# Performance work log

Measured on AMD Instinct MI355X. Metric: run time of the kernel, lower is better.

The kernel has to match this reference:

```python
import jax, jax.numpy as jnp
import numpy as np
import math

HIDDEN = 1024
HEADS = 16
HEAD_DIM = HIDDEN // HEADS
B, S = 2, 2048


def _xavier(key, shape):
    fan_in, fan_out = shape[1], shape[0]
    limit = math.sqrt(6.0 / (fan_in + fan_out))
    return jax.random.uniform(key, shape, jnp.float32, -limit, limit)


def setup_inputs() -> dict:
    key = jax.random.key(0)
    ks = jax.random.split(key, 5)
    x = jax.random.normal(ks[0], (B, S, HIDDEN), jnp.float32)
    # torch Linear stores weight as [out, in]; y = x @ W.T + b
    Wq = _xavier(ks[1], (HIDDEN, HIDDEN))
    Wk = _xavier(ks[2], (HIDDEN, HIDDEN))
    Wv = _xavier(ks[3], (HIDDEN, HIDDEN))
    Wo = _xavier(ks[4], (HIDDEN, HIDDEN))
    bq = jnp.zeros((HIDDEN,), jnp.float32)
    bk = jnp.zeros((HIDDEN,), jnp.float32)
    bv = jnp.zeros((HIDDEN,), jnp.float32)
    bo = jnp.zeros((HIDDEN,), jnp.float32)
    return {"x": x, "Wq": Wq, "bq": bq, "Wk": Wk, "bk": bk,
            "Wv": Wv, "bv": bv, "Wo": Wo, "bo": bo}


def reference(x, Wq, bq, Wk, bk, Wv, bv, Wo, bo):
    b, s, d = x.shape
    h, hd = HEADS, HEAD_DIM
    q = (x @ Wq.T + bq).reshape(b, s, h, hd).transpose(0, 2, 1, 3)  # [b,h,s,hd]
    k = (x @ Wk.T + bk).reshape(b, s, h, hd).transpose(0, 2, 1, 3)
    v = (x @ Wv.T + bv).reshape(b, s, h, hd).transpose(0, 2, 1, 3)
    scores = jnp.einsum('bhqd,bhkd->bhqk', q, k) / math.sqrt(hd)
    causal = jnp.tril(jnp.ones((s, s), bool))
    scores = jnp.where(causal, scores, -jnp.inf)
    attn = jax.nn.softmax(scores, axis=-1)
    out = jnp.einsum('bhqk,bhkd->bhqd', attn, v)  # [b,h,s,hd]
    out = out.transpose(0, 2, 1, 3).reshape(b, s, d)
    return out @ Wo.T + bo
```

## Files before the change

### kernel.cpp

```cpp
#include <hip/hip_runtime.h>
#include <hip/hip_bf16.h>


typedef __hip_bfloat16 bf16;
typedef __attribute__((ext_vector_type(8))) short short8;
typedef __attribute__((ext_vector_type(4))) short short4v;
typedef __attribute__((ext_vector_type(4))) float f32x4;

#define MFMA16(a, b, c) __builtin_amdgcn_mfma_f32_16x16x32_bf16((a), (b), (c), 0, 0, 0)

__device__ __forceinline__ void load_lds16(const void* g, void* l) {
  __builtin_amdgcn_global_load_lds(
      (const __attribute__((address_space(1))) void*)g,
      (__attribute__((address_space(3))) void*)l, 16, 0, 0);
}

__global__ __launch_bounds__(256) void cvt_kernel(
    const float* __restrict__ x, const float* __restrict__ wq,
    const float* __restrict__ wk, const float* __restrict__ wv,
    const float* __restrict__ wo, bf16* __restrict__ xb, bf16* __restrict__ wqb,
    bf16* __restrict__ wkb, bf16* __restrict__ wvb, bf16* __restrict__ wob) {
  const int seg = blockIdx.y;
  const float* src;
  bf16* dst;
  int n;
  if (seg == 0)      { src = x;  dst = xb;  n = 4194304; }
  else if (seg == 1) { src = wq; dst = wqb; n = 1048576; }
  else if (seg == 2) { src = wk; dst = wkb; n = 1048576; }
  else if (seg == 3) { src = wv; dst = wvb; n = 1048576; }
  else               { src = wo; dst = wob; n = 1048576; }
  const int i = (blockIdx.x * 256 + threadIdx.x) * 4;
  if (i >= n) return;
  const float4 v = *(const float4*)(src + i);
  short4v p;
  ((bf16*)&p)[0] = __float2bfloat16(v.x);
  ((bf16*)&p)[1] = __float2bfloat16(v.y);
  ((bf16*)&p)[2] = __float2bfloat16(v.z);
  ((bf16*)&p)[3] = __float2bfloat16(v.w);
  *(short4v*)(dst + i) = p;
}

template <typename OutT>
__device__ __forceinline__ void gemm_body(const bf16* __restrict__ X,
                                          const bf16* __restrict__ W,
                                          const float* __restrict__ bias,
                                          OutT* __restrict__ Y, float scale) {
  constexpr int K = 1024, N = 1024;
  __shared__ bf16 As[128 * 32];
  __shared__ bf16 Bs[128 * 32];
  const int t = threadIdx.x;
  const int lane = t & 63, w = t >> 6;
  const int quad = lane >> 4, r = lane & 15;
  const int m0 = blockIdx.y * 128, n0 = blockIdx.x * 128;
  const int wm = w >> 1, wn = w & 1;

  f32x4 acc[4][4] = {};

  for (int k0 = 0; k0 < K; k0 += 32) {
    __syncthreads();
#pragma unroll
    for (int p = 0; p < 2; ++p) {
      const int c = p * 256 + w * 64 + lane;
      const int row = c >> 2;
      const int scb = (c & 3) ^ ((row >> 1) & 3);
      load_lds16(X + (size_t)(m0 + row) * K + k0 + scb * 8,
                 As + (p * 256 + w * 64) * 8);
      load_lds16(W + (size_t)(n0 + row) * K + k0 + scb * 8,
                 Bs + (p * 256 + w * 64) * 8);
    }
    __syncthreads();
    short8 af[4], bfr[4];
#pragma unroll
    for (int i = 0; i < 4; ++i) {
      const int ra = wm * 64 + i * 16 + r;
      af[i] = *(const short8*)(As + ra * 32 + ((quad ^ ((ra >> 1) & 3)) * 8));
      const int rb = wn * 64 + i * 16 + r;
      bfr[i] = *(const short8*)(Bs + rb * 32 + ((quad ^ ((rb >> 1) & 3)) * 8));
    }
#pragma unroll
    for (int i = 0; i < 4; ++i)
#pragma unroll
      for (int j = 0; j < 4; ++j)
        acc[i][j] = MFMA16(af[i], bfr[j], acc[i][j]);
  }
#pragma unroll
  for (int i = 0; i < 4; ++i) {
    const int m = m0 + wm * 64 + i * 16 + quad * 4;
#pragma unroll
    for (int j = 0; j < 4; ++j) {
      const int n = n0 + wn * 64 + j * 16 + r;
      const float bv = bias[n];
#pragma unroll
      for (int g = 0; g < 4; ++g) {
        const float val = (acc[i][j][g] + bv) * scale;
        if constexpr (__is_same(OutT, float))
          Y[(size_t)(m + g) * N + n] = val;
        else
          Y[(size_t)(m + g) * N + n] = __float2bfloat16(val);
      }
    }
  }
}

__global__ __launch_bounds__(256) void qkv_kernel(
    const bf16* __restrict__ x, const bf16* __restrict__ Wq,
    const float* __restrict__ bq, const bf16* __restrict__ Wk,
    const float* __restrict__ bk, const bf16* __restrict__ Wv,
    const float* __restrict__ bv, bf16* Qb, bf16* Kb, bf16* Vb) {
  const bf16* W;
  const float* bias;
  bf16* Y;
  float scale = 1.0f;
  if (blockIdx.z == 0) { W = Wq; bias = bq; Y = Qb; scale = 0.125f; }
  else if (blockIdx.z == 1) { W = Wk; bias = bk; Y = Kb; }
  else { W = Wv; bias = bv; Y = Vb; }
  gemm_body<bf16>(x, W, bias, Y, scale);
}

__global__ __launch_bounds__(256) void proj_kernel(const bf16* __restrict__ X,
                                                   const bf16* __restrict__ W,
                                                   const float* __restrict__ bias,
                                                   float* __restrict__ Y) {
  gemm_body<float>(X, W, bias, Y, 1.0f);
}

__global__ __launch_bounds__(256) void attn_kernel(const bf16* __restrict__ Qb,
                                                   const bf16* __restrict__ Kb,
                                                   const bf16* __restrict__ Vb,
                                                   bf16* __restrict__ Ob) {
  const int pair = blockIdx.x, h = blockIdx.y, b = blockIdx.z;
  const int t = threadIdx.x;
  const int lane = t & 63, w = t >> 6;
  const int quad = lane >> 4, r = lane & 15;

  __shared__ bf16 Ks[64 * 64];
  __shared__ bf16 Vt[64 * 64];
  __shared__ bf16 Pl[4][16 * 64];

#pragma unroll 1
  for (int sel = 0; sel < 2; ++sel) {
    const int j = sel ? (31 - pair) : pair;
    const int q0 = j * 64;
    const int qrow = q0 + w * 16 + r;

    short8 qf[2];
#pragma unroll
    for (int ks = 0; ks < 2; ++ks)
      qf[ks] = *(const short8*)(Qb + (size_t)(b * 2048 + qrow) * 1024 + h * 64 +
                                ks * 32 + quad * 8);

    f32x4 o[4] = {};
    float mrow = -1e30f, lrow = 0.f;

    for (int kt = 0; kt <= j; ++kt) {
      const int k0 = kt * 64;
      __syncthreads();
#pragma unroll
      for (int p = 0; p < 2; ++p) {
        const int c = p * 256 + w * 64 + lane;
        const int row = c >> 3;
        const int scb = (c & 7) ^ (row & 7);
        load_lds16(Kb + (size_t)(b * 2048 + k0 + row) * 1024 + h * 64 + scb * 8,
                   Ks + (p * 256 + w * 64) * 8);
      }
      {
        const bf16* vsrc =
            Vb + (size_t)(b * 2048 + k0 + lane) * 1024 + h * 64 + w * 16;
        short8 v0 = *(const short8*)(vsrc);
        short8 v1 = *(const short8*)(vsrc + 8);
        const int s8 = lane >> 3, s7 = lane & 7;
#pragma unroll
        for (int jj = 0; jj < 8; ++jj) {
          const int d0 = w * 16 + jj, d1 = w * 16 + 8 + jj;
          Vt[d0 * 64 + ((s8 ^ jj) * 8) + s7] = ((const bf16*)&v0)[jj];
          Vt[d1 * 64 + ((s8 ^ jj) * 8) + s7] = ((const bf16*)&v1)[jj];
        }
      }
      __syncthreads();

      f32x4 st[4] = {};
#pragma unroll
      for (int ks = 0; ks < 2; ++ks) {
        short8 kf[4];
#pragma unroll
        for (int mt = 0; mt < 4; ++mt) {
          const int key = mt * 16 + r;
          kf[mt] = *(const short8*)(Ks + key * 64 +
                                    (((ks * 4 + quad) ^ (key & 7)) * 8));
        }
#pragma unroll
        for (int mt = 0; mt < 4; ++mt) st[mt] = MFMA16(kf[mt], qf[ks], st[mt]);
      }

      if (kt == j) {
#pragma unroll
        for (int mt = 0; mt < 4; ++mt)
#pragma unroll
          for (int g = 0; g < 4; ++g) {
            const int key = k0 + mt * 16 + quad * 4 + g;
            if (key > qrow) st[mt][g] = -1e30f;
          }
      }

      float mx = -1e30f;
#pragma unroll
      for (int mt = 0; mt < 4; ++mt)
#pragma unroll
        for (int g = 0; g < 4; ++g) mx = fmaxf(mx, st[mt][g]);
      mx = fmaxf(mx, __shfl_xor(mx, 16));
      mx = fmaxf(mx, __shfl_xor(mx, 32));
      const float mnew = fmaxf(mrow, mx);
      const float alpha = __expf(mrow - mnew);
      mrow = mnew;
      float sum = 0.f;
#pragma unroll
      for (int mt = 0; mt < 4; ++mt) {
        bf16 pk[4];
#pragma unroll
        for (int g = 0; g < 4; ++g) {
          const float p = __expf(st[mt][g] - mnew);
          pk[g] = __float2bfloat16(p);
          sum += __bfloat162float(pk[g]);
        }
        const int key8 = mt * 2 + (quad >> 1);
        const int off = r * 64 + ((key8 ^ (r & 7)) * 8) + (quad & 1) * 4;
        *(short4v*)(&Pl[w][off]) = *(const short4v*)pk;
      }
      sum += __shfl_xor(sum, 16);
      sum += __shfl_xor(sum, 32);
      lrow = lrow * alpha + sum;
#pragma unroll
      for (int mt = 0; mt < 4; ++mt)
#pragma unroll
        for (int g = 0; g < 4; ++g) o[mt][g] *= alpha;

      asm volatile("s_waitcnt lgkmcnt(0)" ::: "memory");

#pragma unroll
      for (int ks = 0; ks < 2; ++ks) {
        short8 vf[4], pf;
#pragma unroll
        for (int mt = 0; mt < 4; ++mt) {
          const int d = mt * 16 + r;
          vf[mt] = *(const short8*)(Vt + d * 64 +
                                    (((ks * 4 + quad) ^ (d & 7)) * 8));
        }
        pf = *(const short8*)(Pl[w] + r * 64 + (((ks * 4 + quad) ^ (r & 7)) * 8));
#pragma unroll
        for (int mt = 0; mt < 4; ++mt) o[mt] = MFMA16(vf[mt], pf, o[mt]);
      }
    }

    const float inv = 1.f / lrow;
#pragma unroll
    for (int mt = 0; mt < 4; ++mt) {
      const int d0 = mt * 16 + quad * 4;
      short4v pk;
#pragma unroll
      for (int g = 0; g < 4; ++g)
        ((bf16*)&pk)[g] = __float2bfloat16(o[mt][g] * inv);
      *(short4v*)(Ob + (size_t)(b * 2048 + qrow) * 1024 + h * 64 + d0) = pk;
    }
  }
}

extern "C" void kernel_launch(void* const* d_in, const int* in_sizes, int n_in,
                              void* d_out, int out_size, void* d_ws, size_t ws_size,
                              hipStream_t stream) {
  const float* x  = (const float*)d_in[0];
  const float* Wq = (const float*)d_in[1];
  const float* bq = (const float*)d_in[2];
  const float* Wk = (const float*)d_in[3];
  const float* bk = (const float*)d_in[4];
  const float* Wv = (const float*)d_in[5];
  const float* bv = (const float*)d_in[6];
  const float* Wo = (const float*)d_in[7];
  const float* bo = (const float*)d_in[8];
  float* out = (float*)d_out;

  bf16* xb  = (bf16*)d_ws;
  bf16* wqb = xb  + (size_t)4096 * 1024;
  bf16* wkb = wqb + (size_t)1024 * 1024;
  bf16* wvb = wkb + (size_t)1024 * 1024;
  bf16* wob = wvb + (size_t)1024 * 1024;
  bf16* Qb  = wob + (size_t)1024 * 1024;
  bf16* Kb  = Qb  + (size_t)4096 * 1024;
  bf16* Vb  = Kb  + (size_t)4096 * 1024;
  bf16* Ob  = Vb  + (size_t)4096 * 1024;
  const size_t need = ((size_t)4096 * 1024 * 5 + (size_t)1024 * 1024 * 4) * 2;
  if (ws_size < need) return;

  cvt_kernel<<<dim3(4096, 5), 256, 0, stream>>>(x, Wq, Wk, Wv, Wo,
                                                xb, wqb, wkb, wvb, wob);
  qkv_kernel<<<dim3(8, 32, 3), 256, 0, stream>>>(xb, wqb, bq, wkb, bk, wvb, bv,
                                                 Qb, Kb, Vb);
  attn_kernel<<<dim3(16, 16, 2), 256, 0, stream>>>(Qb, Kb, Vb, Ob);
  proj_kernel<<<dim3(8, 32, 1), 256, 0, stream>>>(Ob, wob, bo, out);
}
```

Measured before the change: 206.3 us.

## Split attention into one block per query tile, shrink proj tile, use exp2

The attention kernel no longer pairs a short and a long causal query tile per block. It launches one block per 64-row tile, heaviest tiles first, which doubles the grid and gives the scheduler finer load balancing. The output projection now uses a 64-row M tile so it launches twice as many blocks. Q is pre-scaled by log2(e)/sqrt(d) so softmax can use exp2f instead of __expf. Each block now does less work, so each block also spends a larger share of its time loading Q and running its prologue.

```diff
diff --git a/kernel.cpp b/kernel.cpp
--- a/kernel.cpp
+++ b/kernel.cpp
@@ -40,52 +40,60 @@
   *(short4v*)(dst + i) = p;
 }
 
-template <typename OutT>
+template <int BM, typename OutT>
 __device__ __forceinline__ void gemm_body(const bf16* __restrict__ X,
                                           const bf16* __restrict__ W,
                                           const float* __restrict__ bias,
                                           OutT* __restrict__ Y, float scale) {
   constexpr int K = 1024, N = 1024;
-  __shared__ bf16 As[128 * 32];
+  constexpr int MI = BM / 32;
+  __shared__ bf16 As[BM * 32];
   __shared__ bf16 Bs[128 * 32];
   const int t = threadIdx.x;
   const int lane = t & 63, w = t >> 6;
   const int quad = lane >> 4, r = lane & 15;
-  const int m0 = blockIdx.y * 128, n0 = blockIdx.x * 128;
+  const int m0 = blockIdx.y * BM, n0 = blockIdx.x * 128;
   const int wm = w >> 1, wn = w & 1;
 
-  f32x4 acc[4][4] = {};
+  f32x4 acc[MI][4] = {};
 
   for (int k0 = 0; k0 < K; k0 += 32) {
     __syncthreads();
+#pragma unroll
+    for (int p = 0; p < BM / 64; ++p) {
+      const int c = p * 256 + w * 64 + lane;
+      const int row = c >> 2;
+      const int scb = (c & 3) ^ ((row >> 1) & 3);
+      load_lds16(X + (size_t)(m0 + row) * K + k0 + scb * 8, As + c * 8);
+    }
 #pragma unroll
     for (int p = 0; p < 2; ++p) {
       const int c = p * 256 + w * 64 + lane;
       const int row = c >> 2;
       const int scb = (c & 3) ^ ((row >> 1) & 3);
-      load_lds16(X + (size_t)(m0 + row) * K + k0 + scb * 8,
-                 As + (p * 256 + w * 64) * 8);
-      load_lds16(W + (size_t)(n0 + row) * K + k0 + scb * 8,
-                 Bs + (p * 256 + w * 64) * 8);
+      load_lds16(W + (size_t)(n0 + row) * K + k0 + scb * 8, Bs + c * 8);
     }
     __syncthreads();
-    short8 af[4], bfr[4];
-#pragma unroll
-    for (int i = 0; i < 4; ++i) {
-      const int ra = wm * 64 + i * 16 + r;
+    short8 af[MI], bfr[4];
+#pragma unroll
+    for (int i = 0; i < MI; ++i) {
+      const int ra = wm * (MI * 16) + i * 16 + r;
       af[i] = *(const short8*)(As + ra * 32 + ((quad ^ ((ra >> 1) & 3)) * 8));
-      const int rb = wn * 64 + i * 16 + r;
-      bfr[i] = *(const short8*)(Bs + rb * 32 + ((quad ^ ((rb >> 1) & 3)) * 8));
-    }
-#pragma unroll
-    for (int i = 0; i < 4; ++i)
+    }
+#pragma unroll
+    for (int j = 0; j < 4; ++j) {
+      const int rb = wn * 64 + j * 16 + r;
+      bfr[j] = *(const short8*)(Bs + rb * 32 + ((quad ^ ((rb >> 1) & 3)) * 8));
+    }
+#pragma unroll
+    for (int i = 0; i < MI; ++i)
 #pragma unroll
       for (int j = 0; j < 4; ++j)
         acc[i][j] = MFMA16(af[i], bfr[j], acc[i][j]);
   }
 #pragma unroll
-  for (int i = 0; i < 4; ++i) {
-    const int m = m0 + wm * 64 + i * 16 + quad * 4;
+  for (int i = 0; i < MI; ++i) {
+    const int m = m0 + wm * (MI * 16) + i * 16 + quad * 4;
 #pragma unroll
     for (int j = 0; j < 4; ++j) {
       const int n = n0 + wn * 64 + j * 16 + r;
@@ -101,6 +109,8 @@
     }
   }
 }
+
+#define QSCALE 0.18033688f
 
 __global__ __launch_bounds__(256) void qkv_kernel(
     const bf16* __restrict__ x, const bf16* __restrict__ Wq,
@@ -111,24 +121,24 @@
   const float* bias;
   bf16* Y;
   float scale = 1.0f;
-  if (blockIdx.z == 0) { W = Wq; bias = bq; Y = Qb; scale = 0.125f; }
+  if (blockIdx.z == 0) { W = Wq; bias = bq; Y = Qb; scale = QSCALE; }
   else if (blockIdx.z == 1) { W = Wk; bias = bk; Y = Kb; }
   else { W = Wv; bias = bv; Y = Vb; }
-  gemm_body<bf16>(x, W, bias, Y, scale);
+  gemm_body<128, bf16>(x, W, bias, Y, scale);
 }
 
 __global__ __launch_bounds__(256) void proj_kernel(const bf16* __restrict__ X,
                                                    const bf16* __restrict__ W,
                                                    const float* __restrict__ bias,
                                                    float* __restrict__ Y) {
-  gemm_body<float>(X, W, bias, Y, 1.0f);
+  gemm_body<64, float>(X, W, bias, Y, 1.0f);
 }
 
 __global__ __launch_bounds__(256) void attn_kernel(const bf16* __restrict__ Qb,
                                                    const bf16* __restrict__ Kb,
                                                    const bf16* __restrict__ Vb,
                                                    bf16* __restrict__ Ob) {
-  const int pair = blockIdx.x, h = blockIdx.y, b = blockIdx.z;
+  const int j = 31 - blockIdx.x, h = blockIdx.y, b = blockIdx.z;
   const int t = threadIdx.x;
   const int lane = t & 63, w = t >> 6;
   const int quad = lane >> 4, r = lane & 15;
@@ -137,130 +147,126 @@
   __shared__ bf16 Vt[64 * 64];
   __shared__ bf16 Pl[4][16 * 64];
 
-#pragma unroll 1
-  for (int sel = 0; sel < 2; ++sel) {
-    const int j = sel ? (31 - pair) : pair;
-    const int q0 = j * 64;
-    const int qrow = q0 + w * 16 + r;
-
-    short8 qf[2];
-#pragma unroll
-    for (int ks = 0; ks < 2; ++ks)
-      qf[ks] = *(const short8*)(Qb + (size_t)(b * 2048 + qrow) * 1024 + h * 64 +
-                                ks * 32 + quad * 8);
-
-    f32x4 o[4] = {};
-    float mrow = -1e30f, lrow = 0.f;
-
-    for (int kt = 0; kt <= j; ++kt) {
-      const int k0 = kt * 64;
-      __syncthreads();
-#pragma unroll
-      for (int p = 0; p < 2; ++p) {
-        const int c = p * 256 + w * 64 + lane;
-        const int row = c >> 3;
-        const int scb = (c & 7) ^ (row & 7);
-        load_lds16(Kb + (size_t)(b * 2048 + k0 + row) * 1024 + h * 64 + scb * 8,
-                   Ks + (p * 256 + w * 64) * 8);
-      }
-      {
-        const bf16* vsrc =
-            Vb + (size_t)(b * 2048 + k0 + lane) * 1024 + h * 64 + w * 16;
-        short8 v0 = *(const short8*)(vsrc);
-        short8 v1 = *(const short8*)(vsrc + 8);
-        const int s8 = lane >> 3, s7 = lane & 7;
-#pragma unroll
-        for (int jj = 0; jj < 8; ++jj) {
-          const int d0 = w * 16 + jj, d1 = w * 16 + 8 + jj;
-          Vt[d0 * 64 + ((s8 ^ jj) * 8) + s7] = ((const bf16*)&v0)[jj];
-          Vt[d1 * 64 + ((s8 ^ jj) * 8) + s7] = ((const bf16*)&v1)[jj];
+  const int q0 = j * 64;
+  const int qrow = q0 + w * 16 + r;
+
+  short8 qf[2];
+#pragma unroll
+  for (int ks = 0; ks < 2; ++ks)
+    qf[ks] = *(const short8*)(Qb + (size_t)(b * 2048 + qrow) * 1024 + h * 64 +
+                              ks * 32 + quad * 8);
+
+  f32x4 o[4] = {};
+  float mrow = -1e30f, lrow = 0.f;
+
+  for (int kt = 0; kt <= j; ++kt) {
+    const int k0 = kt * 64;
+    __syncthreads();
+#pragma unroll
+    for (int p = 0; p < 2; ++p) {
+      const int c = p * 256 + w * 64 + lane;
+      const int row = c >> 3;
+      const int scb = (c & 7) ^ (row & 7);
+      load_lds16(Kb + (size_t)(b * 2048 + k0 + row) * 1024 + h * 64 + scb * 8,
+                 Ks + (p * 256 + w * 64) * 8);
+    }
+    {
+      const bf16* vsrc =
+          Vb + (size_t)(b * 2048 + k0 + lane) * 1024 + h * 64 + w * 16;
+      short8 v0 = *(const short8*)(vsrc);
+      short8 v1 = *(const short8*)(vsrc + 8);
+      const int s8 = lane >> 3, s7 = lane & 7;
+#pragma unroll
+      for (int jj = 0; jj < 8; ++jj) {
+        const int d0 = w * 16 + jj, d1 = w * 16 + 8 + jj;
+        Vt[d0 * 64 + ((s8 ^ jj) * 8) + s7] = ((const bf16*)&v0)[jj];
+        Vt[d1 * 64 + ((s8 ^ jj) * 8) + s7] = ((const bf16*)&v1)[jj];
+      }
+    }
+    __syncthreads();
+
+    f32x4 st[4] = {};
+#pragma unroll
+    for (int ks = 0; ks < 2; ++ks) {
+      short8 kf[4];
+#pragma unroll
+      for (int mt = 0; mt < 4; ++mt) {
+        const int key = mt * 16 + r;
+        kf[mt] = *(const short8*)(Ks + key * 64 +
+                                  (((ks * 4 + quad) ^ (key & 7)) * 8));
+      }
+#pragma unroll
+      for (int mt = 0; mt < 4; ++mt) st[mt] = MFMA16(kf[mt], qf[ks], st[mt]);
+    }
+
+    if (kt == j) {
+#pragma unroll
+      for (int mt = 0; mt < 4; ++mt)
+#pragma unroll
+        for (int g = 0; g < 4; ++g) {
+          const int key = k0 + mt * 16 + quad * 4 + g;
+          if (key > qrow) st[mt][g] = -1e30f;
         }
-      }
-      __syncthreads();
-
-      f32x4 st[4] = {};
-#pragma unroll
-      for (int ks = 0; ks < 2; ++ks) {
-        short8 kf[4];
-#pragma unroll
-        for (int mt = 0; mt < 4; ++mt) {
-          const int key = mt * 16 + r;
-          kf[mt] = *(const short8*)(Ks + key * 64 +
-                                    (((ks * 4 + quad) ^ (key & 7)) * 8));
-        }
-#pragma unroll
-        for (int mt = 0; mt < 4; ++mt) st[mt] = MFMA16(kf[mt], qf[ks], st[mt]);
-      }
-
-      if (kt == j) {
-#pragma unroll
-        for (int mt = 0; mt < 4; ++mt)
-#pragma unroll
-          for (int g = 0; g < 4; ++g) {
-            const int key = k0 + mt * 16 + quad * 4 + g;
-            if (key > qrow) st[mt][g] = -1e30f;
-          }
-      }
-
-      float mx = -1e30f;
-#pragma unroll
-      for (int mt = 0; mt < 4; ++mt)
-#pragma unroll
-        for (int g = 0; g < 4; ++g) mx = fmaxf(mx, st[mt][g]);
-      mx = fmaxf(mx, __shfl_xor(mx, 16));
-      mx = fmaxf(mx, __shfl_xor(mx, 32));
-      const float mnew = fmaxf(mrow, mx);
-      const float alpha = __expf(mrow - mnew);
-      mrow = mnew;
-      float sum = 0.f;
+    }
+
+    float mx = -1e30f;
+#pragma unroll
+    for (int mt = 0; mt < 4; ++mt)
+#pragma unroll
+      for (int g = 0; g < 4; ++g) mx = fmaxf(mx, st[mt][g]);
+    mx = fmaxf(mx, __shfl_xor(mx, 16));
+    mx = fmaxf(mx, __shfl_xor(mx, 32));
+    const float mnew = fmaxf(mrow, mx);
+    const float alpha = exp2f(mrow - mnew);
+    mrow = mnew;
+    float sum = 0.f;
+#pragma unroll
+    for (int mt = 0; mt < 4; ++mt) {
+      bf16 pk[4];
+#pragma unroll
+      for (int g = 0; g < 4; ++g) {
+        const float p = exp2f(st[mt][g] - mnew);
+        pk[g] = __float2bfloat16(p);
+        sum += __bfloat162float(pk[g]);
+      }
+      const int key8 = mt * 2 + (quad >> 1);
+      const int off = r * 64 + ((key8 ^ (r & 7)) * 8) + (quad & 1) * 4;
+      *(short4v*)(&Pl[w][off]) = *(const short4v*)pk;
+    }
+    sum += __shfl_xor(sum, 16);
+    sum += __shfl_xor(sum, 32);
+    lrow = lrow * alpha + sum;
+#pragma unroll
+    for (int mt = 0; mt < 4; ++mt)
+#pragma unroll
+      for (int g = 0; g < 4; ++g) o[mt][g] *= alpha;
+
+    asm volatile("s_waitcnt lgkmcnt(0)" ::: "memory");
+
+#pragma unroll
+    for (int ks = 0; ks < 2; ++ks) {
+      short8 vf[4], pf;
 #pragma unroll
       for (int mt = 0; mt < 4; ++mt) {
-        bf16 pk[4];
-#pragma unroll
-        for (int g = 0; g < 4; ++g) {
-          const float p = __expf(st[mt][g] - mnew);
-          pk[g] = __float2bfloat16(p);
-          sum += __bfloat162float(pk[g]);
-        }
-        const int key8 = mt * 2 + (quad >> 1);
-        const int off = r * 64 + ((key8 ^ (r & 7)) * 8) + (quad & 1) * 4;
-        *(short4v*)(&Pl[w][off]) = *(const short4v*)pk;
-      }
-      sum += __shfl_xor(sum, 16);
-      sum += __shfl_xor(sum, 32);
-      lrow = lrow * alpha + sum;
-#pragma unroll
-      for (int mt = 0; mt < 4; ++mt)
-#pragma unroll
-        for (int g = 0; g < 4; ++g) o[mt][g] *= alpha;
-
-      asm volatile("s_waitcnt lgkmcnt(0)" ::: "memory");
-
-#pragma unroll
-      for (int ks = 0; ks < 2; ++ks) {
-        short8 vf[4], pf;
-#pragma unroll
-        for (int mt = 0; mt < 4; ++mt) {
-          const int d = mt * 16 + r;
-          vf[mt] = *(const short8*)(Vt + d * 64 +
-                                    (((ks * 4 + quad) ^ (d & 7)) * 8));
-        }
-        pf = *(const short8*)(Pl[w] + r * 64 + (((ks * 4 + quad) ^ (r & 7)) * 8));
-#pragma unroll
-        for (int mt = 0; mt < 4; ++mt) o[mt] = MFMA16(vf[mt], pf, o[mt]);
-      }
-    }
-
-    const float inv = 1.f / lrow;
-#pragma unroll
-    for (int mt = 0; mt < 4; ++mt) {
-      const int d0 = mt * 16 + quad * 4;
-      short4v pk;
-#pragma unroll
-      for (int g = 0; g < 4; ++g)
-        ((bf16*)&pk)[g] = __float2bfloat16(o[mt][g] * inv);
-      *(short4v*)(Ob + (size_t)(b * 2048 + qrow) * 1024 + h * 64 + d0) = pk;
-    }
+        const int d = mt * 16 + r;
+        vf[mt] = *(const short8*)(Vt + d * 64 +
+                                  (((ks * 4 + quad) ^ (d & 7)) * 8));
+      }
+      pf = *(const short8*)(Pl[w] + r * 64 + (((ks * 4 + quad) ^ (r & 7)) * 8));
+#pragma unroll
+      for (int mt = 0; mt < 4; ++mt) o[mt] = MFMA16(vf[mt], pf, o[mt]);
+    }
+  }
+
+  const float inv = 1.f / lrow;
+#pragma unroll
+  for (int mt = 0; mt < 4; ++mt) {
+    const int d0 = mt * 16 + quad * 4;
+    short4v pk;
+#pragma unroll
+    for (int g = 0; g < 4; ++g)
+      ((bf16*)&pk)[g] = __float2bfloat16(o[mt][g] * inv);
+    *(short4v*)(Ob + (size_t)(b * 2048 + qrow) * 1024 + h * 64 + d0) = pk;
   }
 }
 
@@ -294,6 +300,6 @@
                                                 xb, wqb, wkb, wvb, wob);
   qkv_kernel<<<dim3(8, 32, 3), 256, 0, stream>>>(xb, wqb, bq, wkb, bk, wvb, bv,
                                                  Qb, Kb, Vb);
-  attn_kernel<<<dim3(16, 16, 2), 256, 0, stream>>>(Qb, Kb, Vb, Ob);
-  proj_kernel<<<dim3(8, 32, 1), 256, 0, stream>>>(Ob, wob, bo, out);
-}
+  attn_kernel<<<dim3(32, 16, 2), 256, 0, stream>>>(Qb, Kb, Vb, Ob);
+  proj_kernel<<<dim3(8, 64, 1), 256, 0, stream>>>(Ob, wob, bo, out);
+}
```

After: 259.3 us. 1.26x slower.
